# Optimization experiments

Measured on AMD Instinct MI355X. Metric: run time of the kernel, lower is better.

## Reference

```python
import jax, jax.numpy as jnp
import numpy as np
from jax import lax

B, T, V, E, H, DA, R, S, A, NR = 256, 64, 30000, 300, 512, 350, 16, 64, 16, 3


def setup_inputs() -> dict:
    key = jax.random.key(0)
    ks = jax.random.split(key, 24)

    def gn(k, shape, scale):
        return (jax.random.normal(k, shape) * scale).astype(jnp.float32)

    def xavier(k, shape):
        fan = sum(shape[-2:]) if len(shape) >= 2 else shape[0] * 2
        return (jax.random.uniform(k, shape, minval=-1.0, maxval=1.0)
                * np.sqrt(6.0 / fan)).astype(jnp.float32)

    s = 1.0 / np.sqrt(H)
    inp = {
        "tokens": jax.random.randint(ks[0], (B, T), 0, V),
        "lengths": jnp.full((B,), T, dtype=jnp.int32),
        "embedding": gn(ks[1], (V, E), 0.02),
        # BiLSTM layer 0 (input E), layer 1 (input 2H); gates order i,f,g,o (PyTorch)
        "Wih_l0f": gn(ks[2], (4 * H, E), s), "Whh_l0f": gn(ks[3], (4 * H, H), s), "b_l0f": jnp.zeros((4 * H,), jnp.float32),
        "Wih_l0b": gn(ks[4], (4 * H, E), s), "Whh_l0b": gn(ks[5], (4 * H, H), s), "b_l0b": jnp.zeros((4 * H,), jnp.float32),
        "Wih_l1f": gn(ks[6], (4 * H, 2 * H), s), "Whh_l1f": gn(ks[7], (4 * H, H), s), "b_l1f": jnp.zeros((4 * H,), jnp.float32),
        "Wih_l1b": gn(ks[8], (4 * H, 2 * H), s), "Whh_l1b": gn(ks[9], (4 * H, H), s), "b_l1b": jnp.zeros((4 * H,), jnp.float32),
        "ws1": xavier(ks[10], (DA, 2 * H)),
        "ws2": xavier(ks[11], (R, DA)),
        "caps_W": xavier(ks[12], (R, 2 * H, S * A)),
    }
    return inp


def _lstm_dir(x, Wih, Whh, b, reverse=False):
    # x: [T, B, D] -> hidden states [T, B, H]
    if reverse:
        x = x[::-1]
    h0 = jnp.zeros((x.shape[1], Whh.shape[1]), x.dtype)
    c0 = jnp.zeros_like(h0)

    def step(carry, xt):
        h, c = carry
        z = xt @ Wih.T + h @ Whh.T + b
        i, f, g, o = jnp.split(z, 4, axis=-1)
        c = jax.nn.sigmoid(f) * c + jax.nn.sigmoid(i) * jnp.tanh(g)
        h = jax.nn.sigmoid(o) * jnp.tanh(c)
        return (h, c), h

    _, hs = lax.scan(step, (h0, c0), x)
    return hs[::-1] if reverse else hs


def reference(tokens, lengths, embedding,
              Wih_l0f, Whh_l0f, b_l0f, Wih_l0b, Whh_l0b, b_l0b,
              Wih_l1f, Whh_l1f, b_l1f, Wih_l1b, Whh_l1b, b_l1b,
              ws1, ws2, caps_W):
    # Embedding + 2-layer BiLSTM (all lengths == T, so packing is a no-op).
    x = embedding[tokens].transpose(1, 0, 2)          # [T, B, E]
    l0 = jnp.concatenate([_lstm_dir(x, Wih_l0f, Whh_l0f, b_l0f),
                          _lstm_dir(x, Wih_l0b, Whh_l0b, b_l0b, True)], -1)
    l1 = jnp.concatenate([_lstm_dir(l0, Wih_l1f, Whh_l1f, b_l1f),
                          _lstm_dir(l0, Wih_l1b, Whh_l1b, b_l1b, True)], -1)
    outp = l1.transpose(1, 0, 2)                      # [B, T, 2H]

    # Self-attention pooling (note: original applies NO softmax on alphas).
    hbar = jnp.tanh(jnp.einsum('bte,ae->bta', outp, ws1))   # [B, T, DA]
    alphas = jnp.einsum('bta,ra->btr', hbar, ws2)           # [B, T, R]
    attention = alphas.transpose(0, 2, 1)                   # [B, R, T]
    sent = jnp.einsum('brt,bte->bre', attention, outp)      # [B, R, 2H]

    # Capsule votes + dynamic routing.
    votes = jnp.einsum('bri,rio->bro', sent, caps_W).reshape(B, R, S, A)
    logits = jnp.zeros((B, R, S), votes.dtype)
    for _ in range(NR):
        route = jax.nn.softmax(logits, axis=2)
        preact = jnp.einsum('brs,brsa->bsa', route, votes)  # [B, S, A]
        norm = jnp.linalg.norm(preact, axis=2, keepdims=True)
        act = preact / norm * (norm * norm / (0.5 + norm * norm))
        logits = logits + jnp.einsum('brsa,bsa->brs', votes, act)
    class_logits = jnp.linalg.norm(act, axis=-1)            # [B, S]
    return (sent, class_logits)
```

## Files before the change

kernel.cpp:

```cpp
#include <hip/hip_runtime.h>
#include <stdint.h>

#define PB 256
#define PT 64
#define PE 300
#define PH 512
#define PDA 350
#define PR 16
#define PS 64
#define PA 16

typedef __attribute__((ext_vector_type(8))) short short8;
typedef __attribute__((ext_vector_type(4))) float f4;
typedef unsigned long long u64;

__device__ __forceinline__ float bf2f(unsigned short u) {
    unsigned v = ((unsigned)u) << 16;
    return __builtin_bit_cast(float, v);
}
__device__ __forceinline__ unsigned short f2bf(float f) {
    unsigned u = __builtin_bit_cast(unsigned int, f);
    u = u + 0x7fffu + ((u >> 16) & 1u);
    return (unsigned short)(u >> 16);
}
__device__ __forceinline__ float sigf(float x) { return 1.f / (1.f + __expf(-x)); }
__device__ __forceinline__ float tanhf_(float x) { return 1.f - 2.f / (1.f + __expf(2.f * x)); }


__global__ __launch_bounds__(256) void k_embed(const int* __restrict__ tokens,
                                               const float* __restrict__ emb,
                                               unsigned short* __restrict__ X) {
    int idx = blockIdx.x * 256 + threadIdx.x;
    if (idx >= 16384 * 320) return;
    int row = idx / 320, e = idx - row * 320;
    int t = row >> 8, b = row & 255;
    float v = 0.f;
    if (e < 300) v = emb[(long)tokens[b * 64 + t] * 300 + e];
    X[idx] = f2bf(v);
}

__global__ __launch_bounds__(256) void k_cvt_pad(const float* __restrict__ src,
                                                 unsigned short* __restrict__ dst,
                                                 int N, int K, int N2, int K2) {
    int idx = blockIdx.x * 256 + threadIdx.x;
    if (idx >= N2 * K2) return;
    int n = idx / K2, k = idx - n * K2;
    float v = (n < N && k < K) ? src[(long)n * K + k] : 0.f;
    dst[idx] = f2bf(v);
}

__global__ __launch_bounds__(256) void k_capsT(const float* __restrict__ src,
                                               unsigned short* __restrict__ dst) {
    __shared__ float tile[32][33];
    int r = blockIdx.x, kb = blockIdx.y * 32, nb = blockIdx.z * 32;
    int tx = threadIdx.x & 31, ty = threadIdx.x >> 5;
    for (int i = 0; i < 32; i += 8)
        tile[ty + i][tx] = src[((long)r << 20) + (long)(kb + ty + i) * 1024 + nb + tx];
    __syncthreads();
    for (int i = 0; i < 32; i += 8)
        dst[((long)r << 20) + (long)(nb + ty + i) * 1024 + kb + tx] = f2bf(tile[tx][ty + i]);
}

__global__ __launch_bounds__(256) void k_whh_shuf(const float* __restrict__ W,
                                                  unsigned short* __restrict__ dst) {
    int idx = blockIdx.x * 256 + threadIdx.x;
    int el = idx & 7, lane = (idx >> 3) & 63, ks = (idx >> 9) & 15, nt = (idx >> 13) & 7, hs = idx >> 16;
    int gcol = (nt >> 1) * 512 + hs * 32 + (nt & 1) * 16 + (lane & 15);
    int k = ks * 32 + (lane >> 4) * 8 + el;
    dst[idx] = f2bf(W[(long)gcol * 512 + k]);
}

template <int OUT_BF16, int TANH>
__global__ __launch_bounds__(256) void k_gemm(const unsigned short* __restrict__ A,
                                              const unsigned short* __restrict__ W,
                                              void* __restrict__ Cv,
                                              const float* __restrict__ bias,
                                              int K, int lda, int ldc,
                                              long aOffZ, long wOffZ, long cOffZ, long bOffZ) {
    A += blockIdx.z * aOffZ;
    W += blockIdx.z * wOffZ;
    if (bias) bias += blockIdx.z * bOffZ;
    const long cbase = blockIdx.z * cOffZ;
    const int m0 = blockIdx.x * 128, n0 = blockIdx.y * 128;
    __shared__ unsigned short As[4096], Bs[4096];
    const int w = threadIdx.x >> 6, l = threadIdx.x & 63;
    const int wm = w & 1, wn = w >> 1;
    const int fr = l & 15, fk = (l >> 4) * 8;
    f4 acc[4][4] = {};
    for (int k0 = 0; k0 < K; k0 += 32) {
        __syncthreads();
#pragma unroll
        for (int i = 0; i < 2; i++) {
            int tI = w + i * 4;
            const unsigned short* ga = A + (long)(m0 + tI * 16 + fr) * lda + k0 + fk;
            const unsigned short* gb = W + (long)(n0 + tI * 16 + fr) * K + k0 + fk;
            *(short8*)&As[tI * 512 + l * 8] = *(const short8*)ga;
            *(short8*)&Bs[tI * 512 + l * 8] = *(const short8*)gb;
        }
        __syncthreads();
        short8 av[4], bv[4];
#pragma unroll
        for (int mt = 0; mt < 4; mt++) av[mt] = *(short8*)&As[(wm * 4 + mt) * 512 + l * 8];
#pragma unroll
        for (int nt = 0; nt < 4; nt++) bv[nt] = *(short8*)&Bs[(wn * 4 + nt) * 512 + l * 8];
#pragma unroll
        for (int mt = 0; mt < 4; mt++)
#pragma unroll
            for (int nt = 0; nt < 4; nt++)
                acc[mt][nt] = __builtin_amdgcn_mfma_f32_16x16x32_bf16(av[mt], bv[nt], acc[mt][nt], 0, 0, 0);
    }
#pragma unroll
    for (int mt = 0; mt < 4; mt++) {
        int row = m0 + wm * 64 + mt * 16 + (l >> 4) * 4;
#pragma unroll
        for (int nt = 0; nt < 4; nt++) {
            int col = n0 + wn * 64 + nt * 16 + (l & 15);
            float bb = bias ? bias[col] : 0.f;
#pragma unroll
            for (int i = 0; i < 4; i++) {
                float v = acc[mt][nt][i] + bb;
                if (TANH) v = tanhf_(v);
                long off = cbase + (long)(row + i) * ldc + col;
                if (OUT_BF16)
                    ((unsigned short*)Cv)[off] = f2bf(v);
                else
                    ((float*)Cv)[off] = v;
            }
        }
    }
}

__global__ __launch_bounds__(256) void k_lstm(const unsigned short* __restrict__ Zx,
                                              const unsigned short* __restrict__ Wshuf,
                                              unsigned short* __restrict__ hsteps,
                                              unsigned short* __restrict__ Lout,
                                              unsigned* __restrict__ cnt) {
    extern __shared__ char smem[];
    unsigned short* Wl = (unsigned short*)smem;
    float* zl = (float*)(smem + 131072);
    const int bid = blockIdx.x;
    const int g = bid & 7, hs = bid >> 3;
    const int dir = g >> 2, bg = g & 3;
    const int tid = threadIdx.x;
    const int l = tid & 63;
    const int w = tid >> 6;
    const int mt2 = w & 1, hc2 = w >> 1;

    {
        const short8* src = (const short8*)(Wshuf + ((long)(dir * 16 + hs) << 16));
        short8* dst = (short8*)Wl;
        for (int i = tid; i < 8192; i += 256) dst[i] = src[i];
    }
    {
        unsigned short* hz = hsteps + (long)dir * (256 * 512);
        for (int i = tid; i < 1024; i += 256) {
            int r = i >> 4, c2 = i & 15;
            __hip_atomic_store((unsigned*)&hz[(bg * 64 + r) * 512 + hs * 32 + c2 * 2], 0u,
                               __ATOMIC_RELAXED, __HIP_MEMORY_SCOPE_AGENT);
        }
    }
    unsigned* myc = cnt + g * 32;
    asm volatile("s_waitcnt vmcnt(0)" ::: "memory");
    __syncthreads();
    if (tid == 0) __hip_atomic_fetch_add(myc, 1u, __ATOMIC_RELAXED, __HIP_MEMORY_SCOPE_AGENT);

    float c_reg[8];
#pragma unroll
    for (int i = 0; i < 8; i++) c_reg[i] = 0.f;

    const int pw_r[2] = { tid >> 4, 16 + (tid >> 4) };
    const int pw_c0 = (tid & 15) * 2;

    for (int step = 0; step < 64; step++) {
        const int t_eff = dir ? (63 - step) : step;
        const unsigned short* zbase = Zx + ((long)dir * 16384 + (long)t_eff * 256) * 2048;

        unsigned zpre[2][2][4];
#pragma unroll
        for (int half = 0; half < 2; half++)
#pragma unroll
            for (int k2 = 0; k2 < 2; k2++) {
                int rowg = bg * 64 + half * 32 + pw_r[k2];
                int jg = hs * 32 + pw_c0;
                const unsigned short* zrow = zbase + (long)rowg * 2048;
#pragma unroll
                for (int gg = 0; gg < 4; gg++)
                    zpre[half][k2][gg] = *(const unsigned*)&zrow[gg * 512 + jg];
            }

        if (tid == 0) {
            unsigned target = 16u * (unsigned)(step + 1);
            while (__hip_atomic_load(myc, __ATOMIC_RELAXED, __HIP_MEMORY_SCOPE_AGENT) < target) {}
        }
        __syncthreads();

        f4 acc[2][4] = {};
        const unsigned short* hb = hsteps + ((long)step * 2 + dir) * (256 * 512);
        const unsigned short* pa0 = hb + (bg * 64 + (mt2 * 2 + 0) * 16 + (l & 15)) * 512 + (l >> 4) * 8;
        const unsigned short* pa1 = hb + (bg * 64 + (mt2 * 2 + 1) * 16 + (l & 15)) * 512 + (l >> 4) * 8;
        short8 a0r[16], a1r[16];
#pragma unroll
        for (int ks = 0; ks < 8; ks++) {
            a0r[ks] = *(const short8*)(pa0 + ks * 32);
            a1r[ks] = *(const short8*)(pa1 + ks * 32);
        }
#pragma unroll
        for (int ks = 0; ks < 16; ks++) {
            if (ks < 8) {
                a0r[ks + 8] = *(const short8*)(pa0 + (ks + 8) * 32);
                a1r[ks + 8] = *(const short8*)(pa1 + (ks + 8) * 32);
            }
#pragma unroll
            for (int s = 0; s < 4; s++) {
                int nt = s * 2 + hc2;
                short8 b = *(short8*)&Wl[((nt * 16 + ks) * 64 + l) * 8];
                acc[0][s] = __builtin_amdgcn_mfma_f32_16x16x32_bf16(a0r[ks], b, acc[0][s], 0, 0, 0);
                acc[1][s] = __builtin_amdgcn_mfma_f32_16x16x32_bf16(a1r[ks], b, acc[1][s], 0, 0, 0);
            }
        }

        unsigned short* hw = hsteps + ((long)(step + 1) * 2 + dir) * (256 * 512);
#pragma unroll
        for (int half = 0; half < 2; half++) {
            __syncthreads();
            if (mt2 == half) {
#pragma unroll
                for (int i2 = 0; i2 < 2; i2++) {
                    int rloc = i2 * 16 + (l >> 4) * 4;
#pragma unroll
                    for (int s = 0; s < 4; s++) {
                        int col = s * 32 + hc2 * 16 + (l & 15);
#pragma unroll
                        for (int i = 0; i < 4; i++) zl[(rloc + i) * 132 + col] = acc[i2][s][i];
                    }
                }
            }
            __syncthreads();
#pragma unroll
            for (int k2 = 0; k2 < 2; k2++) {
                int r = pw_r[k2];
                int c0 = pw_c0;
                int rowg = bg * 64 + half * 32 + r;
                int jg = hs * 32 + c0;
                unsigned ui = zpre[half][k2][0], uf = zpre[half][k2][1];
                unsigned ug = zpre[half][k2][2], uo = zpre[half][k2][3];
                float zi0 = zl[r * 132 + 0 * 32 + c0] + bf2f((unsigned short)ui);
                float zf0 = zl[r * 132 + 1 * 32 + c0] + bf2f((unsigned short)uf);
                float zg0 = zl[r * 132 + 2 * 32 + c0] + bf2f((unsigned short)ug);
                float zo0 = zl[r * 132 + 3 * 32 + c0] + bf2f((unsigned short)uo);
                float zi1 = zl[r * 132 + 0 * 32 + c0 + 1] + bf2f((unsigned short)(ui >> 16));
                float zf1 = zl[r * 132 + 1 * 32 + c0 + 1] + bf2f((unsigned short)(uf >> 16));
                float zg1 = zl[r * 132 + 2 * 32 + c0 + 1] + bf2f((unsigned short)(ug >> 16));
                float zo1 = zl[r * 132 + 3 * 32 + c0 + 1] + bf2f((unsigned short)(uo >> 16));
                int ci = half * 4 + k2 * 2;
                float ca = sigf(zf0) * c_reg[ci] + sigf(zi0) * tanhf_(zg0);
                c_reg[ci] = ca;
                float ha = sigf(zo0) * tanhf_(ca);
                float cb = sigf(zf1) * c_reg[ci + 1] + sigf(zi1) * tanhf_(zg1);
                c_reg[ci + 1] = cb;
                float hbv = sigf(zo1) * tanhf_(cb);
                unsigned pack = (unsigned)f2bf(ha) | ((unsigned)f2bf(hbv) << 16);
                __hip_atomic_store((unsigned*)&hw[(long)rowg * 512 + jg], pack,
                                   __ATOMIC_RELAXED, __HIP_MEMORY_SCOPE_AGENT);
                *(unsigned*)&Lout[((long)t_eff * 256 + rowg) * 1024 + dir * 512 + jg] = pack;
            }
        }
        asm volatile("s_waitcnt vmcnt(0)" ::: "memory");
        __syncthreads();
        if (tid == 0) __hip_atomic_fetch_add(myc, 1u, __ATOMIC_RELAXED, __HIP_MEMORY_SCOPE_AGENT);
    }
}

__global__ __launch_bounds__(256) void k_alphas(const unsigned short* __restrict__ hbar,
                                                const unsigned short* __restrict__ ws2,
                                                float* __restrict__ att) {
    int w = threadIdx.x >> 6, l = threadIdx.x & 63;
    int mtile = blockIdx.x * 4 + w;
    f4 acc = {};
    const unsigned short* arow = hbar + (long)(mtile * 16 + (l & 15)) * 384 + (l >> 4) * 8;
    const unsigned short* brow = ws2 + (long)(l & 15) * 384 + (l >> 4) * 8;
    for (int ks = 0; ks < 12; ks++) {
        short8 a = *(const short8*)&arow[ks * 32];
        short8 b = *(const short8*)&brow[ks * 32];
        acc = __builtin_amdgcn_mfma_f32_16x16x32_bf16(a, b, acc, 0, 0, 0);
    }
    int r = l & 15;
#pragma unroll
    for (int i = 0; i < 4; i++) {
        int bt = mtile * 16 + (l >> 4) * 4 + i;
        int b = bt & 255, t = bt >> 8;
        att[((long)b * 16 + r) * 64 + t] = acc[i];
    }
}

__global__ __launch_bounds__(256) void k_sent(const float* __restrict__ att,
                                              const unsigned short* __restrict__ L1,
                                              float* __restrict__ sent,
                                              unsigned short* __restrict__ sentb) {
    int b = blockIdx.x, n0 = blockIdx.y * 128;
    __shared__ float al[1024];
    for (int i = threadIdx.x; i < 1024; i += 256) al[i] = att[(long)b * 1024 + i];
    __syncthreads();
    int n = n0 + (threadIdx.x & 127);
    int rh = (threadIdx.x >> 7) * 8;
    float acc[8] = {};
    for (int t = 0; t < 64; t++) {
        float x = bf2f(L1[((long)t * 256 + b) * 1024 + n]);
#pragma unroll
        for (int r = 0; r < 8; r++) acc[r] += al[(rh + r) * 64 + t] * x;
    }
#pragma unroll
    for (int r = 0; r < 8; r++) {
        long o = ((long)b * 16 + rh + r) * 1024 + n;
        sent[o] = acc[r];
        sentb[o] = f2bf(acc[r]);
    }
}

__global__ __launch_bounds__(256) void k_route(const float* __restrict__ votes,
                                               float* __restrict__ clog) {
    __shared__ float v[16384];
    __shared__ float logits[1024];
    __shared__ float route[1024];
    __shared__ float pre[1024];
    __shared__ float act[1024];
    __shared__ float cl[64];
    int b = blockIdx.x, tid = threadIdx.x;
    for (int i = tid; i < 4096; i += 256) ((f4*)v)[i] = ((const f4*)(votes + (long)b * 16384))[i];
    for (int i = tid; i < 1024; i += 256) logits[i] = 0.f;
    __syncthreads();
    for (int it = 0; it < 3; it++) {
        if (tid < 16) {
            float m = -1e30f;
            for (int s = 0; s < 64; s++) m = fmaxf(m, logits[tid * 64 + s]);
            float sum = 0.f;
            for (int s = 0; s < 64; s++) {
                float e = __expf(logits[tid * 64 + s] - m);
                route[tid * 64 + s] = e;
                sum += e;
            }
            float inv = 1.f / sum;
            for (int s = 0; s < 64; s++) route[tid * 64 + s] *= inv;
        }
        __syncthreads();
#pragma unroll
        for (int k = 0; k < 4; k++) {
            int p = k * 256 + tid;
            int s = p >> 4, a = p & 15;
            float acc = 0.f;
            for (int r = 0; r < 16; r++) acc += route[r * 64 + s] * v[(r * 64 + s) * 16 + a];
            pre[p] = acc;
        }
        __syncthreads();
        if (tid < 64) {
            float nsq = 0.f;
            for (int a = 0; a < 16; a++) nsq += pre[tid * 16 + a] * pre[tid * 16 + a];
            float norm = sqrtf(nsq);
            float sc = norm / (0.5f + nsq);
            for (int a = 0; a < 16; a++) act[tid * 16 + a] = pre[tid * 16 + a] * sc;
            cl[tid] = nsq / (0.5f + nsq);
        }
        __syncthreads();
#pragma unroll
        for (int k = 0; k < 4; k++) {
            int p = k * 256 + tid;
            int r = p >> 6, s = p & 63;
            float acc = 0.f;
            for (int a = 0; a < 16; a++) acc += v[(r * 64 + s) * 16 + a] * act[s * 16 + a];
            logits[p] += acc;
        }
        __syncthreads();
    }
    if (tid < 64) clog[(long)b * 64 + tid] = cl[tid];
}

extern "C" void kernel_launch(void* const* d_in, const int* in_sizes, int n_in,
                              void* d_out, int out_size, void* d_ws, size_t ws_size,
                              hipStream_t stream) {
    const int* tokens = (const int*)d_in[0];
    const float* embedding = (const float*)d_in[2];
    const float* Wih_l0f = (const float*)d_in[3];
    const float* Whh_l0f = (const float*)d_in[4];
    const float* b_l0f = (const float*)d_in[5];
    const float* Wih_l0b = (const float*)d_in[6];
    const float* Whh_l0b = (const float*)d_in[7];
    const float* b_l0b = (const float*)d_in[8];
    const float* Wih_l1f = (const float*)d_in[9];
    const float* Whh_l1f = (const float*)d_in[10];
    const float* b_l1f = (const float*)d_in[11];
    const float* Wih_l1b = (const float*)d_in[12];
    const float* Whh_l1b = (const float*)d_in[13];
    const float* b_l1b = (const float*)d_in[14];
    const float* ws1 = (const float*)d_in[15];
    const float* ws2 = (const float*)d_in[16];
    const float* caps_W = (const float*)d_in[17];
    float* out = (float*)d_out;

    char* ws = (char*)d_ws;
    size_t o = 0;
    unsigned short* Xb16 = (unsigned short*)(ws + o); o += (size_t)16384 * 320 * 2;
    unsigned short* ZxL = (unsigned short*)(ws + o); size_t zx_off = o; o += (size_t)2 * 16384 * 2048 * 2;
    unsigned short* L0 = (unsigned short*)(ws + o); o += (size_t)16384 * 1024 * 2;
    unsigned short* L1 = (unsigned short*)(ws + o); o += (size_t)16384 * 1024 * 2;
    unsigned short* Wl0b = (unsigned short*)(ws + o); o += (size_t)2 * 2048 * 320 * 2;
    unsigned short* Wl1b = (unsigned short*)(ws + o); o += (size_t)2 * 2048 * 1024 * 2;
    unsigned short* Wsh0 = (unsigned short*)(ws + o); o += (size_t)2 * 1048576 * 2;
    unsigned short* Wsh1 = (unsigned short*)(ws + o); o += (size_t)2 * 1048576 * 2;
    unsigned short* ws1b = (unsigned short*)(ws + o); o += (size_t)384 * 1024 * 2;
    unsigned short* ws2b = (unsigned short*)(ws + o); o += (size_t)16 * 384 * 2 + 192;
    float* biasc = (float*)(ws + o); o += (size_t)4 * 2048 * 4;
    unsigned* cnts = (unsigned*)(ws + o); o += 4096;
    unsigned short* hsteps = (unsigned short*)(ws + o);
    unsigned short* capsT = (unsigned short*)(ws + o);
    o += (size_t)65 * 2 * 256 * 512 * 2;
    unsigned short* hbarb = (unsigned short*)(ws + zx_off);
    float* att = (float*)(ws + zx_off + (size_t)16384 * 384 * 2);
    unsigned short* sentb = (unsigned short*)(ws + zx_off + (size_t)16384 * 384 * 2 + 1048576);
    float* votes = (float*)(ws + zx_off + (size_t)16384 * 384 * 2 + 1048576 + (size_t)256 * 16 * 1024 * 2);

    hipMemsetAsync(cnts, 0, 4096, stream);

    k_embed<<<16384 * 320 / 256, 256, 0, stream>>>(tokens, embedding, Xb16);
    k_cvt_pad<<<(2048 * 320 + 255) / 256, 256, 0, stream>>>(Wih_l0f, Wl0b, 2048, 300, 2048, 320);
    k_cvt_pad<<<(2048 * 320 + 255) / 256, 256, 0, stream>>>(Wih_l0b, Wl0b + (size_t)2048 * 320, 2048, 300, 2048, 320);
    k_cvt_pad<<<(2048 * 1024 + 255) / 256, 256, 0, stream>>>(Wih_l1f, Wl1b, 2048, 1024, 2048, 1024);
    k_cvt_pad<<<(2048 * 1024 + 255) / 256, 256, 0, stream>>>(Wih_l1b, Wl1b + (size_t)2048 * 1024, 2048, 1024, 2048, 1024);
    k_cvt_pad<<<(384 * 1024 + 255) / 256, 256, 0, stream>>>(ws1, ws1b, 350, 1024, 384, 1024);
    k_cvt_pad<<<(16 * 384 + 255) / 256, 256, 0, stream>>>(ws2, ws2b, 16, 350, 16, 384);
    k_whh_shuf<<<4096, 256, 0, stream>>>(Whh_l0f, Wsh0);
    k_whh_shuf<<<4096, 256, 0, stream>>>(Whh_l0b, Wsh0 + 1048576);
    k_whh_shuf<<<4096, 256, 0, stream>>>(Whh_l1f, Wsh1);
    k_whh_shuf<<<4096, 256, 0, stream>>>(Whh_l1b, Wsh1 + 1048576);
    hipMemcpyAsync(biasc + 0, b_l0f, 2048 * 4, hipMemcpyDeviceToDevice, stream);
    hipMemcpyAsync(biasc + 2048, b_l0b, 2048 * 4, hipMemcpyDeviceToDevice, stream);
    hipMemcpyAsync(biasc + 4096, b_l1f, 2048 * 4, hipMemcpyDeviceToDevice, stream);
    hipMemcpyAsync(biasc + 6144, b_l1b, 2048 * 4, hipMemcpyDeviceToDevice, stream);

    hipFuncSetAttribute(reinterpret_cast<const void*>(k_lstm),
                        hipFuncAttributeMaxDynamicSharedMemorySize, 147968);

    k_gemm<1, 0><<<dim3(128, 16, 2), 256, 0, stream>>>(
        Xb16, Wl0b, ZxL, biasc, 320, 320, 2048,
        0L, (long)2048 * 320, (long)16384 * 2048, 2048L);
    k_lstm<<<128, 256, 147968, stream>>>(ZxL, Wsh0, hsteps, L0, cnts);
    k_gemm<1, 0><<<dim3(128, 16, 2), 256, 0, stream>>>(
        L0, Wl1b, ZxL, biasc + 4096, 1024, 1024, 2048,
        0L, (long)2048 * 1024, (long)16384 * 2048, 2048L);
    k_lstm<<<128, 256, 147968, stream>>>(ZxL, Wsh1, hsteps, L1, cnts + 256);
    k_capsT<<<dim3(16, 32, 32), 256, 0, stream>>>(caps_W, capsT);
    k_gemm<1, 1><<<dim3(128, 3, 1), 256, 0, stream>>>(
        L1, ws1b, hbarb, nullptr, 1024, 1024, 384, 0L, 0L, 0L, 0L);
    k_alphas<<<256, 256, 0, stream>>>(hbarb, ws2b, att);
    k_sent<<<dim3(256, 8), 256, 0, stream>>>(att, L1, out, sentb);
    k_gemm<0, 0><<<dim3(2, 8, 16), 256, 0, stream>>>(
        sentb, capsT, votes, nullptr, 1024, 16384, 16384,
        1024L, 1048576L, 1024L, 0L);
    k_route<<<256, 256, 0, stream>>>(votes, out + (size_t)4194304);
}
```

Measured before the change: 1.698 ms.

## Compute LSTM gate epilogue directly from MFMA accumulators, dropping LDS round-trip

The recurrent LSTM kernel now applies the gate nonlinearities directly on the MFMA accumulator layout, since each lane already holds all four gates for its own rows and columns. This removes the shared-memory staging buffer and the four barriers per step that went with it. The gate preactivation prefetch is reorganised to match that layout, all h operand loads are issued up front, and the Lout store is moved after the counter signal so it is off the critical path. The trade-off is 16-bit scattered global loads and stores (including 16-bit atomic stores of h) in place of the previous packed 32-bit accesses.

```diff
diff --git a/kernel.cpp b/kernel.cpp
--- a/kernel.cpp
+++ b/kernel.cpp
@@ -130,14 +130,13 @@
     }
 }
 
-__global__ __launch_bounds__(256) void k_lstm(const unsigned short* __restrict__ Zx,
-                                              const unsigned short* __restrict__ Wshuf,
-                                              unsigned short* __restrict__ hsteps,
-                                              unsigned short* __restrict__ Lout,
-                                              unsigned* __restrict__ cnt) {
+__global__ __launch_bounds__(256, 1) void k_lstm(const unsigned short* __restrict__ Zx,
+                                                 const unsigned short* __restrict__ Wshuf,
+                                                 unsigned short* __restrict__ hsteps,
+                                                 unsigned short* __restrict__ Lout,
+                                                 unsigned* __restrict__ cnt) {
     extern __shared__ char smem[];
     unsigned short* Wl = (unsigned short*)smem;
-    float* zl = (float*)(smem + 131072);
     const int bid = blockIdx.x;
     const int g = bid & 7, hs = bid >> 3;
     const int dir = g >> 2, bg = g & 3;
@@ -168,24 +167,21 @@
 #pragma unroll
     for (int i = 0; i < 8; i++) c_reg[i] = 0.f;
 
-    const int pw_r[2] = { tid >> 4, 16 + (tid >> 4) };
-    const int pw_c0 = (tid & 15) * 2;
+    const int colg = hs * 32 + hc2 * 16 + (l & 15);
+    const int rbase = bg * 64 + mt2 * 32 + (l >> 4) * 4;
 
     for (int step = 0; step < 64; step++) {
         const int t_eff = dir ? (63 - step) : step;
         const unsigned short* zbase = Zx + ((long)dir * 16384 + (long)t_eff * 256) * 2048;
 
-        unsigned zpre[2][2][4];
-#pragma unroll
-        for (int half = 0; half < 2; half++)
-#pragma unroll
-            for (int k2 = 0; k2 < 2; k2++) {
-                int rowg = bg * 64 + half * 32 + pw_r[k2];
-                int jg = hs * 32 + pw_c0;
-                const unsigned short* zrow = zbase + (long)rowg * 2048;
-#pragma unroll
-                for (int gg = 0; gg < 4; gg++)
-                    zpre[half][k2][gg] = *(const unsigned*)&zrow[gg * 512 + jg];
+        unsigned short zpre[2][4][4];
+#pragma unroll
+        for (int i2 = 0; i2 < 2; i2++)
+#pragma unroll
+            for (int i = 0; i < 4; i++) {
+                const unsigned short* zrow = zbase + (long)(rbase + i2 * 16 + i) * 2048 + colg;
+#pragma unroll
+                for (int s = 0; s < 4; s++) zpre[i2][i][s] = zrow[s * 512];
             }
 
         if (tid == 0) {
@@ -195,21 +191,17 @@
         __syncthreads();
 
         f4 acc[2][4] = {};
-        const unsigned short* hb = hsteps + ((long)step * 2 + dir) * (256 * 512);
-        const unsigned short* pa0 = hb + (bg * 64 + (mt2 * 2 + 0) * 16 + (l & 15)) * 512 + (l >> 4) * 8;
-        const unsigned short* pa1 = hb + (bg * 64 + (mt2 * 2 + 1) * 16 + (l & 15)) * 512 + (l >> 4) * 8;
+        const unsigned short* hbp = hsteps + ((long)step * 2 + dir) * (256 * 512);
+        const unsigned short* pa0 = hbp + (bg * 64 + (mt2 * 2 + 0) * 16 + (l & 15)) * 512 + (l >> 4) * 8;
+        const unsigned short* pa1 = hbp + (bg * 64 + (mt2 * 2 + 1) * 16 + (l & 15)) * 512 + (l >> 4) * 8;
         short8 a0r[16], a1r[16];
 #pragma unroll
-        for (int ks = 0; ks < 8; ks++) {
+        for (int ks = 0; ks < 16; ks++) {
             a0r[ks] = *(const short8*)(pa0 + ks * 32);
             a1r[ks] = *(const short8*)(pa1 + ks * 32);
         }
 #pragma unroll
         for (int ks = 0; ks < 16; ks++) {
-            if (ks < 8) {
-                a0r[ks + 8] = *(const short8*)(pa0 + (ks + 8) * 32);
-                a1r[ks + 8] = *(const short8*)(pa1 + (ks + 8) * 32);
-            }
 #pragma unroll
             for (int s = 0; s < 4; s++) {
                 int nt = s * 2 + hc2;
@@ -220,54 +212,32 @@
         }
 
         unsigned short* hw = hsteps + ((long)(step + 1) * 2 + dir) * (256 * 512);
-#pragma unroll
-        for (int half = 0; half < 2; half++) {
-            __syncthreads();
-            if (mt2 == half) {
-#pragma unroll
-                for (int i2 = 0; i2 < 2; i2++) {
-                    int rloc = i2 * 16 + (l >> 4) * 4;
-#pragma unroll
-                    for (int s = 0; s < 4; s++) {
-                        int col = s * 32 + hc2 * 16 + (l & 15);
-#pragma unroll
-                        for (int i = 0; i < 4; i++) zl[(rloc + i) * 132 + col] = acc[i2][s][i];
-                    }
-                }
+        unsigned short hv[2][4];
+#pragma unroll
+        for (int i2 = 0; i2 < 2; i2++)
+#pragma unroll
+            for (int i = 0; i < 4; i++) {
+                float zi = acc[i2][0][i] + bf2f(zpre[i2][i][0]);
+                float zf = acc[i2][1][i] + bf2f(zpre[i2][i][1]);
+                float zg = acc[i2][2][i] + bf2f(zpre[i2][i][2]);
+                float zo = acc[i2][3][i] + bf2f(zpre[i2][i][3]);
+                int ci = i2 * 4 + i;
+                float cc = sigf(zf) * c_reg[ci] + sigf(zi) * tanhf_(zg);
+                c_reg[ci] = cc;
+                float hh = sigf(zo) * tanhf_(cc);
+                unsigned short h16 = f2bf(hh);
+                hv[i2][i] = h16;
+                __hip_atomic_store(&hw[(long)(rbase + i2 * 16 + i) * 512 + colg], h16,
+                                   __ATOMIC_RELAXED, __HIP_MEMORY_SCOPE_AGENT);
             }
-            __syncthreads();
-#pragma unroll
-            for (int k2 = 0; k2 < 2; k2++) {
-                int r = pw_r[k2];
-                int c0 = pw_c0;
-                int rowg = bg * 64 + half * 32 + r;
-                int jg = hs * 32 + c0;
-                unsigned ui = zpre[half][k2][0], uf = zpre[half][k2][1];
-                unsigned ug = zpre[half][k2][2], uo = zpre[half][k2][3];
-                float zi0 = zl[r * 132 + 0 * 32 + c0] + bf2f((unsigned short)ui);
-                float zf0 = zl[r * 132 + 1 * 32 + c0] + bf2f((unsigned short)uf);
-                float zg0 = zl[r * 132 + 2 * 32 + c0] + bf2f((unsigned short)ug);
-                float zo0 = zl[r * 132 + 3 * 32 + c0] + bf2f((unsigned short)uo);
-                float zi1 = zl[r * 132 + 0 * 32 + c0 + 1] + bf2f((unsigned short)(ui >> 16));
-                float zf1 = zl[r * 132 + 1 * 32 + c0 + 1] + bf2f((unsigned short)(uf >> 16));
-                float zg1 = zl[r * 132 + 2 * 32 + c0 + 1] + bf2f((unsigned short)(ug >> 16));
-                float zo1 = zl[r * 132 + 3 * 32 + c0 + 1] + bf2f((unsigned short)(uo >> 16));
-                int ci = half * 4 + k2 * 2;
-                float ca = sigf(zf0) * c_reg[ci] + sigf(zi0) * tanhf_(zg0);
-                c_reg[ci] = ca;
-                float ha = sigf(zo0) * tanhf_(ca);
-                float cb = sigf(zf1) * c_reg[ci + 1] + sigf(zi1) * tanhf_(zg1);
-                c_reg[ci + 1] = cb;
-                float hbv = sigf(zo1) * tanhf_(cb);
-                unsigned pack = (unsigned)f2bf(ha) | ((unsigned)f2bf(hbv) << 16);
-                __hip_atomic_store((unsigned*)&hw[(long)rowg * 512 + jg], pack,
-                                   __ATOMIC_RELAXED, __HIP_MEMORY_SCOPE_AGENT);
-                *(unsigned*)&Lout[((long)t_eff * 256 + rowg) * 1024 + dir * 512 + jg] = pack;
-            }
-        }
         asm volatile("s_waitcnt vmcnt(0)" ::: "memory");
         __syncthreads();
         if (tid == 0) __hip_atomic_fetch_add(myc, 1u, __ATOMIC_RELAXED, __HIP_MEMORY_SCOPE_AGENT);
+#pragma unroll
+        for (int i2 = 0; i2 < 2; i2++)
+#pragma unroll
+            for (int i = 0; i < 4; i++)
+                Lout[((long)t_eff * 256 + rbase + i2 * 16 + i) * 1024 + dir * 512 + colg] = hv[i2][i];
     }
 }
 
@@ -437,16 +407,16 @@
     hipMemcpyAsync(biasc + 6144, b_l1b, 2048 * 4, hipMemcpyDeviceToDevice, stream);
 
     hipFuncSetAttribute(reinterpret_cast<const void*>(k_lstm),
-                        hipFuncAttributeMaxDynamicSharedMemorySize, 147968);
+                        hipFuncAttributeMaxDynamicSharedMemorySize, 131072);
 
     k_gemm<1, 0><<<dim3(128, 16, 2), 256, 0, stream>>>(
         Xb16, Wl0b, ZxL, biasc, 320, 320, 2048,
         0L, (long)2048 * 320, (long)16384 * 2048, 2048L);
-    k_lstm<<<128, 256, 147968, stream>>>(ZxL, Wsh0, hsteps, L0, cnts);
+    k_lstm<<<128, 256, 131072, stream>>>(ZxL, Wsh0, hsteps, L0, cnts);
     k_gemm<1, 0><<<dim3(128, 16, 2), 256, 0, stream>>>(
         L0, Wl1b, ZxL, biasc + 4096, 1024, 1024, 2048,
         0L, (long)2048 * 1024, (long)16384 * 2048, 2048L);
-    k_lstm<<<128, 256, 147968, stream>>>(ZxL, Wsh1, hsteps, L1, cnts + 256);
+    k_lstm<<<128, 256, 131072, stream>>>(ZxL, Wsh1, hsteps, L1, cnts + 256);
     k_capsT<<<dim3(16, 32, 32), 256, 0, stream>>>(caps_W, capsT);
     k_gemm<1, 1><<<dim3(128, 3, 1), 256, 0, stream>>>(
         L1, ws1b, hbarb, nullptr, 1024, 1024, 384, 0L, 0L, 0L, 0L);
```

Result: no change. 1.706 ms (+0.5%).
